# Kernel tuning notes

Hardware: AMD Instinct MI355X
Metric: run time of the kernel (lower is better)

## Reference

```python
import jax, jax.numpy as jnp
import numpy as np

B_, N_, H_ = 512, 32, 128     # batch, max atoms, edge hidden dim
K_, PSTEPS_ = 3, 10           # low-rank approx rank, power-iteration steps
T_ = 100                      # total_time gradient-descent iterations
EPS_D = 0.01                  # euclidean-distance regularizer (tsg_eps)
EPS_SPEED = 1e-3              # speed regularizer (tsg_eps2)
LR = 0.1                      # tsg_eps1 step size
ALPHA, ALPHA_BASE = 5.0, 0.1  # tanh trust-region schedule


def setup_inputs() -> dict:
    key = jax.random.key(0)
    ks = jax.random.split(key, 6)
    return {
        "gnn_edge_out": jax.random.normal(ks[0], (B_, N_, N_, H_), jnp.float32),
        "W1": jax.random.normal(ks[1], (H_, H_), jnp.float32) * 0.05,
        "b1": jnp.zeros((H_,), jnp.float32),
        "W2": jax.random.normal(ks[2], (H_, 2), jnp.float32) * 0.05,
        "b2": jnp.zeros((2,), jnp.float32),
        "noise": jax.random.normal(ks[3], (B_, N_, 3), jnp.float32),
        "u_init": jax.random.normal(ks[4], (K_, B_, N_, 1), jnp.float32),
    }


def _dist_weights(e, W1, b1, W2, b2):
    # DistWeightLayer: MLP over edge features, symmetrize, softplus -> (D_init, W)
    h = jax.nn.relu(jnp.einsum("bijh,hk->bijk", e, W1) + b1)
    out = jnp.einsum("bijh,hk->bijk", h, W2) + b2           # [B,N,N,2]
    out = out + jnp.swapaxes(out, 1, 2)                      # symmetrize over atom axes
    mask = 1.0 - jnp.eye(N_, dtype=out.dtype)
    D_init = jax.nn.softplus(out[..., 0]) * mask             # zero diagonal
    W = jax.nn.softplus(out[..., 1])
    return D_init, W


def _low_rank_approx_power(A, u_init):
    # rank-K_ power iteration with deflation; A: [B,N,N]
    u_set = []
    A_lr = A
    for i in range(K_):
        u = u_init[i]                                        # [B,N,1]
        for _ in range(PSTEPS_):
            nrm = jnp.linalg.norm(u, axis=1, keepdims=True)  # F.normalize(dim=1, eps=1e-3)
            u = u / jnp.maximum(nrm, 1e-3)
            u = jnp.matmul(A_lr, u)
        eig_sq = jnp.sum(u * u, axis=1, keepdims=True)       # [B,1,1]
        u = u * jnp.power(eig_sq + 0.01, 0.25)               # u / (eig+eps)^-0.25
        u_set.append(u)
        A_lr = A_lr - jnp.matmul(u, jnp.swapaxes(u, 1, 2))
    return jnp.concatenate(u_set, axis=-1)                   # [B,N,3]


def _dist_nlsq(D, W, noise, u_init):
    G = jnp.matmul(jnp.swapaxes(D, 1, 2), D)                 # dist_to_gram: D^T D
    X0 = _low_rank_approx_power(G, u_init) + noise           # [B,N,3]

    def energy(X):
        diff = X[:, :, None, :] - X[:, None, :, :]           # [B,N,N,3]
        D_X = jnp.sqrt(jnp.sum(diff * diff, -1) + EPS_D)
        return jnp.sum(W * jnp.square(D - D_X))

    grad_e = jax.grad(energy)

    def step(X, t):
        dX = -LR * grad_e(X)                                 # [B,N,3]
        speed = jnp.sqrt(jnp.sum(dX * dX, -1) + EPS_SPEED)   # [B,N]
        a_t = ALPHA_BASE + (ALPHA - ALPHA_BASE) * ((T_ - t) / T_)
        scale = a_t * jnp.tanh(speed / a_t) / speed
        return X + dX * scale[..., None], None

    Xf, _ = jax.lax.scan(step, X0, jnp.arange(T_, dtype=X0.dtype))
    return Xf


def reference(gnn_edge_out, W1, b1, W2, b2, noise, u_init):
    D_init, W = _dist_weights(gnn_edge_out, W1, b1, W2, b2)
    X_pred = _dist_nlsq(D_init, W, noise, u_init)
    return (D_init, W, X_pred)
```

## Files before the change

### kernel.cpp

```cpp
#include <hip/hip_runtime.h>
#include <math.h>

#define B_    512
#define N_    32
#define H_    128
#define KRANK 3
#define PSTEPS 10
#define TSTEPS 100

typedef __attribute__((ext_vector_type(4))) float f32x4;
typedef __attribute__((ext_vector_type(8))) short bf16x8;
typedef __attribute__((ext_vector_type(4))) unsigned short u16x4;

__device__ __forceinline__ unsigned short bf16_rne(float x) {
    unsigned int u = __float_as_uint(x);
    u += 0x7FFFu + ((u >> 16) & 1u);
    return (unsigned short)(u >> 16);
}

__device__ __forceinline__ float tanh_pos_fast(float x) {
    float e = __expf(2.f * x);
    return 1.f - 2.f * __builtin_amdgcn_rcpf(e + 1.f);
}

__global__ void kprep_w(const float* __restrict__ W1, unsigned short* __restrict__ Wpk) {
    int t = blockIdx.x * 256 + threadIdx.x;
    int lane = t & 63, nf = (t >> 6) & 7, bk = t >> 9;
    int n = nf * 16 + (lane & 15);
    int kbase = (bk & 3) * 32 + (lane >> 4) * 8;
    u16x4 o0, o1;
    #pragma unroll
    for (int i = 0; i < 8; ++i) {
        float w = W1[(kbase + i) * H_ + n];
        unsigned short hi = bf16_rne(w);
        unsigned short v;
        if (bk < 4) v = hi;
        else        v = bf16_rne(w - __uint_as_float((unsigned int)hi << 16));
        if (i < 4) o0[i] = v; else o1[i - 4] = v;
    }
    u16x4* dst = (u16x4*)(Wpk + (long)t * 8);
    dst[0] = o0;
    dst[1] = o1;
}

#define PADJ 136
__global__ __launch_bounds__(128, 1) void k1_mlp(
    const float* __restrict__ e, const unsigned short* __restrict__ Wpk,
    const float* __restrict__ b1, const float* __restrict__ W2,
    const float* __restrict__ b2,
    float* __restrict__ r0, float* __restrict__ r1) {

    __shared__ __attribute__((aligned(16))) unsigned short Ahi[64 * PADJ];
    __shared__ __attribute__((aligned(16))) unsigned short Alo[64 * PADJ];

    int tid = threadIdx.x;
    long ebase = (long)blockIdx.x * 64;

    #pragma unroll
    for (int it = 0; it < 16; ++it) {
        int flat = it * 128 + tid;
        int row = flat >> 5, col4 = flat & 31;
        f32x4 v = *(const f32x4*)(e + (ebase + row) * H_ + col4 * 4);
        u16x4 hi4, lo4;
        #pragma unroll
        for (int q = 0; q < 4; ++q) {
            unsigned short h = bf16_rne(v[q]);
            hi4[q] = h;
            lo4[q] = bf16_rne(v[q] - __uint_as_float((unsigned int)h << 16));
        }
        *(u16x4*)&Ahi[row * PADJ + col4 * 4] = hi4;
        *(u16x4*)&Alo[row * PADJ + col4 * 4] = lo4;
    }
    __syncthreads();

    int lane = tid & 63, wv = tid >> 6;
    int mrow = lane & 15, khalf = lane >> 4;

    float b1v[8];
    #pragma unroll
    for (int nf = 0; nf < 8; ++nf) b1v[nf] = b1[nf * 16 + mrow];

    f32x4 acc[2][8];
    #pragma unroll
    for (int mf = 0; mf < 2; ++mf)
        #pragma unroll
        for (int nf = 0; nf < 8; ++nf)
            acc[mf][nf] = (f32x4){b1v[nf], b1v[nf], b1v[nf], b1v[nf]};

    #pragma unroll 2
    for (int kk = 0; kk < 12; ++kk) {
        const unsigned short* ab = (kk >= 4 && kk < 8) ? Alo : Ahi;
        int kin = (kk & 3) * 32 + khalf * 8;
        int bk  = (kk < 4) ? kk : kk - 4;
        bf16x8 bfr[8];
        #pragma unroll
        for (int nf = 0; nf < 8; ++nf)
            bfr[nf] = *(const bf16x8*)(Wpk + (((bk * 8 + nf) * 64 + lane) * 8));
        #pragma unroll
        for (int mf = 0; mf < 2; ++mf) {
            bf16x8 av = *(const bf16x8*)&ab[(wv * 32 + mf * 16 + mrow) * PADJ + kin];
            #pragma unroll
            for (int nf = 0; nf < 8; ++nf)
                acc[mf][nf] = __builtin_amdgcn_mfma_f32_16x16x32_bf16(
                    av, bfr[nf], acc[mf][nf], 0, 0, 0);
        }
    }

    float w2a[8], w2b[8];
    #pragma unroll
    for (int nf = 0; nf < 8; ++nf) {
        int j = nf * 16 + mrow;
        w2a[nf] = W2[j * 2];
        w2b[nf] = W2[j * 2 + 1];
    }
    float bb0 = b2[0], bb1 = b2[1];
    #pragma unroll
    for (int mf = 0; mf < 2; ++mf) {
        #pragma unroll
        for (int r = 0; r < 4; ++r) {
            float p0 = 0.f, p1 = 0.f;
            #pragma unroll
            for (int nf = 0; nf < 8; ++nf) {
                float hv = fmaxf(acc[mf][nf][r], 0.f);
                p0 = fmaf(hv, w2a[nf], p0);
                p1 = fmaf(hv, w2b[nf], p1);
            }
            #pragma unroll
            for (int d = 1; d < 16; d <<= 1) {
                p0 += __shfl_xor(p0, d);
                p1 += __shfl_xor(p1, d);
            }
            if (mrow == 0) {
                long edge = ebase + wv * 32 + mf * 16 + khalf * 4 + r;
                r0[edge] = p0 + bb0;
                r1[edge] = p1 + bb1;
            }
        }
    }
}

__device__ __forceinline__ float softplusf(float x) {
    return x > 20.f ? x : log1pf(expf(x));
}

__global__ void k2_sym(float* __restrict__ r0, float* __restrict__ r1) {
    int t = blockIdx.x * 256 + threadIdx.x;
    int b = t / 528, r = t % 528;
    float disc = sqrtf((float)(4225 - 8 * r));
    int i = (int)((65.f - disc) * 0.5f);
    int j = r - (i * (65 - i)) / 2 + i;
    int base = b * 1024;
    int ij = base + i * 32 + j;
    int ji = base + j * 32 + i;
    float s0 = r0[ij] + r0[ji];
    float s1 = r1[ij] + r1[ji];
    float Dv = (i == j) ? 0.f : softplusf(s0);
    float Wv = softplusf(s1);
    r0[ij] = Dv; r0[ji] = Dv;
    r1[ij] = Wv; r1[ji] = Wv;
}

__global__ __launch_bounds__(128) void k3_solve(
    const float* __restrict__ Dg, const float* __restrict__ Wg,
    const float* __restrict__ noise, const float* __restrict__ u_init,
    float* __restrict__ Xout) {
    int b = blockIdx.x;
    int tid = threadIdx.x;

    __shared__ float Ds[32][33];
    __shared__ float Ws_[32][33];
    __shared__ float Gs[32][33];
    __shared__ float Xb[2][32][5];

    const float* Db = Dg + b * 1024;
    const float* Wb = Wg + b * 1024;
    #pragma unroll 1
    for (int s = 0; s < 8; ++s) {
        int idx = s * 128 + tid;
        int i = idx >> 5, j = idx & 31;
        Ds[i][j]  = Db[idx];
        Ws_[i][j] = Wb[idx];
    }
    __syncthreads();

    #pragma unroll 1
    for (int s = 0; s < 8; ++s) {
        int idx = s * 128 + tid;
        int i = idx >> 5, j = idx & 31;
        float acc = 0.f;
        #pragma unroll
        for (int k = 0; k < 32; ++k) acc = fmaf(Ds[k][i], Ds[k][j], acc);
        Gs[i][j] = acc;
    }
    __syncthreads();

    int w = tid >> 6, lane = tid & 63;
    int il = lane & 15;
    int i = w * 16 + il;
    int jq = lane >> 4;
    float Drow[8], Wrow[8];
    #pragma unroll
    for (int jj = 0; jj < 8; ++jj) {
        int j = jq * 8 + jj;
        Drow[jj] = Ds[i][j];
        Wrow[jj] = Ws_[i][j];
    }

    if (tid < 32) {
        int l = tid;
        float Arow[32];
        #pragma unroll
        for (int j = 0; j < 32; ++j) Arow[j] = Gs[l][j];
        float x0 = 0.f, x1 = 0.f, x2 = 0.f;
        for (int s = 0; s < KRANK; ++s) {
            float u = u_init[((long)s * B_ + b) * 32 + l];
            for (int p = 0; p < PSTEPS; ++p) {
                float red = u * u;
                #pragma unroll
                for (int m = 1; m < 32; m <<= 1) red += __shfl_xor(red, m, 32);
                float un = u * __builtin_amdgcn_rcpf(fmaxf(__builtin_amdgcn_sqrtf(red), 1e-3f));
                float acc = 0.f;
                #pragma unroll
                for (int j = 0; j < 32; ++j) acc = fmaf(Arow[j], __shfl(un, j, 32), acc);
                u = acc;
            }
            float red = u * u;
            #pragma unroll
            for (int m = 1; m < 32; m <<= 1) red += __shfl_xor(red, m, 32);
            float sc = __builtin_amdgcn_sqrtf(__builtin_amdgcn_sqrtf(red + 0.01f));
            u *= sc;
            if (s == 0) x0 = u; else if (s == 1) x1 = u; else x2 = u;
            #pragma unroll
            for (int j = 0; j < 32; ++j) Arow[j] = fmaf(-u, __shfl(u, j, 32), Arow[j]);
        }
        const float* nb = noise + ((long)b * 32 + l) * 3;
        Xb[0][l][0] = x0 + nb[0];
        Xb[0][l][1] = x1 + nb[1];
        Xb[0][l][2] = x2 + nb[2];
    }
    __syncthreads();

    #pragma unroll 1
    for (int t = 0; t < TSTEPS; ++t) {
        int rb = t & 1;
        float a_t = 0.1f + 4.9f * (float)(TSTEPS - t) / (float)TSTEPS;
        float ra  = __builtin_amdgcn_rcpf(a_t);
        float xi0 = Xb[rb][i][0], xi1 = Xb[rb][i][1], xi2 = Xb[rb][i][2];
        float sc_ = 0.f, s0 = 0.f, s1 = 0.f, s2 = 0.f;
        #pragma unroll
        for (int jj = 0; jj < 8; ++jj) {
            int j = jq * 8 + jj;
            float xj0 = Xb[rb][j][0], xj1 = Xb[rb][j][1], xj2 = Xb[rb][j][2];
            float dx = xi0 - xj0, dy = xi1 - xj1, dz = xi2 - xj2;
            float dd = fmaf(dx, dx, fmaf(dy, dy, fmaf(dz, dz, 0.01f)));
            float c = -4.f * Wrow[jj] * fmaf(Drow[jj], __builtin_amdgcn_rsqf(dd), -1.f);
            sc_ += c;
            s0 = fmaf(c, xj0, s0);
            s1 = fmaf(c, xj1, s1);
            s2 = fmaf(c, xj2, s2);
        }
        sc_ += __shfl_xor(sc_, 16); s0 += __shfl_xor(s0, 16);
        s1  += __shfl_xor(s1, 16);  s2 += __shfl_xor(s2, 16);
        sc_ += __shfl_xor(sc_, 32); s0 += __shfl_xor(s0, 32);
        s1  += __shfl_xor(s1, 32);  s2 += __shfl_xor(s2, 32);
        if (jq == 0) {
            float d0 = -0.1f * fmaf(xi0, sc_, -s0);
            float d1 = -0.1f * fmaf(xi1, sc_, -s1);
            float d2 = -0.1f * fmaf(xi2, sc_, -s2);
            float sd = fmaf(d0, d0, fmaf(d1, d1, fmaf(d2, d2, 1e-3f)));
            float rs = __builtin_amdgcn_rsqf(sd);
            float arg = sd * rs * ra;
            float scale = a_t * tanh_pos_fast(arg) * rs;
            Xb[rb ^ 1][i][0] = fmaf(d0, scale, xi0);
            Xb[rb ^ 1][i][1] = fmaf(d1, scale, xi1);
            Xb[rb ^ 1][i][2] = fmaf(d2, scale, xi2);
        }
        __syncthreads();
    }

    if (tid < 32) {
        float* xo = Xout + ((long)b * 32 + tid) * 3;
        xo[0] = Xb[0][tid][0];
        xo[1] = Xb[0][tid][1];
        xo[2] = Xb[0][tid][2];
    }
}

extern "C" void kernel_launch(void* const* d_in, const int* in_sizes, int n_in,
                              void* d_out, int out_size, void* d_ws, size_t ws_size,
                              hipStream_t stream) {
    const float* e      = (const float*)d_in[0];
    const float* W1     = (const float*)d_in[1];
    const float* b1     = (const float*)d_in[2];
    const float* W2     = (const float*)d_in[3];
    const float* b2     = (const float*)d_in[4];
    const float* noise  = (const float*)d_in[5];
    const float* u_init = (const float*)d_in[6];
    float* out = (float*)d_out;

    unsigned short* Wpk = (unsigned short*)d_ws;

    float* r0 = out;
    float* r1 = out + 524288;
    float* X  = out + 1048576;

    hipLaunchKernelGGL(kprep_w, dim3(16),   dim3(256), 0, stream, W1, Wpk);
    hipLaunchKernelGGL(k1_mlp,  dim3(8192), dim3(128), 0, stream, e, Wpk, b1, W2, b2, r0, r1);
    hipLaunchKernelGGL(k2_sym,  dim3(1056), dim3(256), 0, stream, r0, r1);
    hipLaunchKernelGGL(k3_solve, dim3(512), dim3(128), 0, stream, r0, r1, noise, u_init, X);
}
```

Baseline: 212.9 us.

## Load edge features directly into MFMA registers, dropping LDS staging in MLP kernel

Measured after the change: 192.8 us. -9.5%, faster.

```diff
diff --git a/kernel.cpp b/kernel.cpp
--- a/kernel.cpp
+++ b/kernel.cpp
@@ -43,67 +43,79 @@
     dst[1] = o1;
 }
 
-#define PADJ 136
-__global__ __launch_bounds__(128, 1) void k1_mlp(
+__global__ __launch_bounds__(256, 2) void k1_mlp(
     const float* __restrict__ e, const unsigned short* __restrict__ Wpk,
     const float* __restrict__ b1, const float* __restrict__ W2,
     const float* __restrict__ b2,
     float* __restrict__ r0, float* __restrict__ r1) {
 
-    __shared__ __attribute__((aligned(16))) unsigned short Ahi[64 * PADJ];
-    __shared__ __attribute__((aligned(16))) unsigned short Alo[64 * PADJ];
-
     int tid = threadIdx.x;
-    long ebase = (long)blockIdx.x * 64;
-
-    #pragma unroll
-    for (int it = 0; it < 16; ++it) {
-        int flat = it * 128 + tid;
-        int row = flat >> 5, col4 = flat & 31;
-        f32x4 v = *(const f32x4*)(e + (ebase + row) * H_ + col4 * 4);
-        u16x4 hi4, lo4;
-        #pragma unroll
-        for (int q = 0; q < 4; ++q) {
-            unsigned short h = bf16_rne(v[q]);
-            hi4[q] = h;
-            lo4[q] = bf16_rne(v[q] - __uint_as_float((unsigned int)h << 16));
-        }
-        *(u16x4*)&Ahi[row * PADJ + col4 * 4] = hi4;
-        *(u16x4*)&Alo[row * PADJ + col4 * 4] = lo4;
-    }
-    __syncthreads();
-
-    int lane = tid & 63, wv = tid >> 6;
-    int mrow = lane & 15, khalf = lane >> 4;
-
-    float b1v[8];
-    #pragma unroll
-    for (int nf = 0; nf < 8; ++nf) b1v[nf] = b1[nf * 16 + mrow];
+    int w = tid >> 6, lane = tid & 63;
+    int mrow = lane & 15, kq = lane >> 4;
+    long ebase = ((long)blockIdx.x * 4 + w) * 32;
+
+    bf16x8 ahi[2][4], alo[2][4];
+    #pragma unroll
+    for (int mf = 0; mf < 2; ++mf) {
+        #pragma unroll
+        for (int kf = 0; kf < 4; ++kf) {
+            const float* ap = e + (ebase + mf * 16 + mrow) * H_ + kf * 32 + kq * 8;
+            f32x4 v0 = *(const f32x4*)ap;
+            f32x4 v1 = *(const f32x4*)(ap + 4);
+            bf16x8 h, l;
+            #pragma unroll
+            for (int q = 0; q < 4; ++q) {
+                unsigned int u0 = __float_as_uint(v0[q]);
+                h[q] = (short)(u0 >> 16);
+                l[q] = (short)bf16_rne(v0[q] - __uint_as_float(u0 & 0xffff0000u));
+                unsigned int u1 = __float_as_uint(v1[q]);
+                h[q + 4] = (short)(u1 >> 16);
+                l[q + 4] = (short)bf16_rne(v1[q] - __uint_as_float(u1 & 0xffff0000u));
+            }
+            ahi[mf][kf] = h;
+            alo[mf][kf] = l;
+        }
+    }
 
     f32x4 acc[2][8];
     #pragma unroll
-    for (int mf = 0; mf < 2; ++mf)
+    for (int nf = 0; nf < 8; ++nf) {
+        float bv = b1[nf * 16 + mrow];
+        acc[0][nf] = (f32x4){bv, bv, bv, bv};
+        acc[1][nf] = acc[0][nf];
+    }
+
+    #pragma unroll
+    for (int kf = 0; kf < 4; ++kf) {
+        bf16x8 bh[8];
         #pragma unroll
         for (int nf = 0; nf < 8; ++nf)
-            acc[mf][nf] = (f32x4){b1v[nf], b1v[nf], b1v[nf], b1v[nf]};
-
-    #pragma unroll 2
-    for (int kk = 0; kk < 12; ++kk) {
-        const unsigned short* ab = (kk >= 4 && kk < 8) ? Alo : Ahi;
-        int kin = (kk & 3) * 32 + khalf * 8;
-        int bk  = (kk < 4) ? kk : kk - 4;
-        bf16x8 bfr[8];
-        #pragma unroll
-        for (int nf = 0; nf < 8; ++nf)
-            bfr[nf] = *(const bf16x8*)(Wpk + (((bk * 8 + nf) * 64 + lane) * 8));
-        #pragma unroll
-        for (int mf = 0; mf < 2; ++mf) {
-            bf16x8 av = *(const bf16x8*)&ab[(wv * 32 + mf * 16 + mrow) * PADJ + kin];
+            bh[nf] = *(const bf16x8*)(Wpk + (((kf * 8 + nf) * 64 + lane) * 8));
+        #pragma unroll
+        for (int mf = 0; mf < 2; ++mf)
             #pragma unroll
             for (int nf = 0; nf < 8; ++nf)
                 acc[mf][nf] = __builtin_amdgcn_mfma_f32_16x16x32_bf16(
-                    av, bfr[nf], acc[mf][nf], 0, 0, 0);
-        }
+                    ahi[mf][kf], bh[nf], acc[mf][nf], 0, 0, 0);
+        #pragma unroll
+        for (int mf = 0; mf < 2; ++mf)
+            #pragma unroll
+            for (int nf = 0; nf < 8; ++nf)
+                acc[mf][nf] = __builtin_amdgcn_mfma_f32_16x16x32_bf16(
+                    alo[mf][kf], bh[nf], acc[mf][nf], 0, 0, 0);
+    }
+    #pragma unroll
+    for (int kf = 0; kf < 4; ++kf) {
+        bf16x8 bl[8];
+        #pragma unroll
+        for (int nf = 0; nf < 8; ++nf)
+            bl[nf] = *(const bf16x8*)(Wpk + ((((4 + kf) * 8 + nf) * 64 + lane) * 8));
+        #pragma unroll
+        for (int mf = 0; mf < 2; ++mf)
+            #pragma unroll
+            for (int nf = 0; nf < 8; ++nf)
+                acc[mf][nf] = __builtin_amdgcn_mfma_f32_16x16x32_bf16(
+                    ahi[mf][kf], bl[nf], acc[mf][nf], 0, 0, 0);
     }
 
     float w2a[8], w2b[8];
@@ -131,7 +143,7 @@
                 p1 += __shfl_xor(p1, d);
             }
             if (mrow == 0) {
-                long edge = ebase + wv * 32 + mf * 16 + khalf * 4 + r;
+                long edge = ebase + mf * 16 + kq * 4 + r;
                 r0[edge] = p0 + bb0;
                 r1[edge] = p1 + bb1;
             }
@@ -305,7 +317,7 @@
     float* X  = out + 1048576;
 
     hipLaunchKernelGGL(kprep_w, dim3(16),   dim3(256), 0, stream, W1, Wpk);
-    hipLaunchKernelGGL(k1_mlp,  dim3(8192), dim3(128), 0, stream, e, Wpk, b1, W2, b2, r0, r1);
+    hipLaunchKernelGGL(k1_mlp,  dim3(4096), dim3(256), 0, stream, e, Wpk, b1, W2, b2, r0, r1);
     hipLaunchKernelGGL(k2_sym,  dim3(1056), dim3(256), 0, stream, r0, r1);
     hipLaunchKernelGGL(k3_solve, dim3(512), dim3(128), 0, stream, r0, r1, noise, u_init, X);
 }
```
